# Optimization experiments

Hardware: AMD Instinct MI355X
Metric: run time of the kernel (lower is better)

The kernel has to match this reference:

```python
import jax, jax.numpy as jnp
import numpy as np

B, SQ, SK, D = 8, 512, 512, 32


def _spd_cov(key, b, s, d):
    # random SPD covariance: A A^T + I
    a = 0.1 * jax.random.normal(key, (b, s, d, d), dtype=jnp.float32)
    return jnp.einsum('bsde,bsfe->bsdf', a, a) + jnp.eye(d, dtype=jnp.float32)


def setup_inputs() -> dict:
    key = jax.random.key(0)
    ks = jax.random.split(key, 6)
    return {
        'q_mean': jax.random.normal(ks[0], (B, SQ, D), dtype=jnp.float32),
        'q_cov': _spd_cov(ks[1], B, SQ, D),
        'k_mean': jax.random.normal(ks[2], (B, SK, D), dtype=jnp.float32),
        'k_cov': _spd_cov(ks[3], B, SK, D),
        'v_mean': jax.random.normal(ks[4], (B, SK, D), dtype=jnp.float32),
        'v_cov': _spd_cov(ks[5], B, SK, D),
    }


def reference(q_mean, q_cov, k_mean, k_cov, v_mean, v_cov):
    # Pairwise symmetric Gaussian JSD attention.
    # JSD = 0.5*(KL(p_q||p_k)+KL(p_k||p_q)); the log-det terms cancel:
    # JSD = 0.25*( tr(Sk^-1 Sq) + tr(Sq^-1 Sk) - 2D
    #              + dm^T (Sk^-1 + Sq^-1) dm ),  dm = mu_q - mu_k
    d = q_mean.shape[-1]
    q_inv = jnp.linalg.inv(q_cov)            # [B,Sq,D,D]
    k_inv = jnp.linalg.inv(k_cov)            # [B,Sk,D,D]
    tr_kq = jnp.einsum('bkde,bqed->bqk', k_inv, q_cov)
    tr_qk = jnp.einsum('bqde,bked->bqk', q_inv, k_cov)
    dm = q_mean[:, :, None, :] - k_mean[:, None, :, :]   # [B,Sq,Sk,D]
    quad = (jnp.einsum('bqkd,bkde,bqke->bqk', dm, k_inv, dm)
            + jnp.einsum('bqkd,bqde,bqke->bqk', dm, q_inv, dm))
    js = 0.25 * (tr_kq + tr_qk - 2.0 * d + quad)         # [B,Sq,Sk]
    score = jax.nn.softmax(js, axis=-1)
    out_mean = jnp.einsum('bqk,bkd->bqd', score, v_mean)
    out_cov = jnp.einsum('bqk,bkde->bqde', score, v_cov)
    return out_mean, out_cov
```

## Files before the change

### kernel.cpp

```cpp
#include <hip/hip_runtime.h>
#include <hip/hip_bf16.h>

#define NBATCH 8
#define SQL 512
#define SKL 512
#define DD 32
#define KF 1152
#define UT 528
#define NOUT 1056
#define NVT 1088
#define NSITE (NBATCH * SQL)
#define VS_BLOCKS (34 * 16 * NBATCH)

typedef short short8 __attribute__((ext_vector_type(8)));
typedef float f32x4 __attribute__((ext_vector_type(4)));
typedef unsigned short ushort_t;

__device__ __forceinline__ ushort_t f2bf(float f) {
    unsigned int u = __float_as_uint(f);
    return (ushort_t)((u + 0x7fffu + ((u >> 16) & 1u)) >> 16);
}
__device__ __forceinline__ float bf2f(ushort_t h) {
    return __uint_as_float(((unsigned int)h) << 16);
}
__device__ __forceinline__ void gl_lds16(const ushort_t* g, ushort_t* l) {
    __builtin_amdgcn_global_load_lds(
        (const __attribute__((address_space(1))) void*)g,
        (__attribute__((address_space(3))) void*)l, 16, 0, 0);
}
__device__ __forceinline__ void pk_split(float v0, float v1, ushort_t& h0, ushort_t& h1,
                                         ushort_t& l0, ushort_t& l1) {
    __hip_bfloat162 H = __float22bfloat162_rn(make_float2(v0, v1));
    ushort2 hu = *(ushort2*)&H;
    h0 = hu.x; h1 = hu.y;
    __hip_bfloat162 L = __float22bfloat162_rn(make_float2(v0 - bf2f(hu.x), v1 - bf2f(hu.y)));
    ushort2 lu = *(ushort2*)&L;
    l0 = lu.x; l1 = lu.y;
}

template<int P>
__device__ __forceinline__ float swzb(float x) {
    return __int_as_float(__builtin_amdgcn_ds_swizzle(__float_as_int(x), (P << 5)));
}
template<int M>
__device__ __forceinline__ float swzx(float x) {
    return __int_as_float(__builtin_amdgcn_ds_swizzle(__float_as_int(x), (M << 10) | 0x1F));
}

template<int P>
__device__ __forceinline__ void gj_step(float (&a)[DD], int hl) {
    float piv = swzb<P>(a[P]);
    float rinv = __builtin_amdgcn_rcpf(piv);
    float t = a[P] * rinv;
    bool isp = (hl == P);
    float u = isp ? rinv : t;
    float g = isp ? 0.0f : 1.0f;
    #pragma unroll
    for (int i = 0; i < DD; ++i) {
        if (i == P) continue;
        float ci = swzb<P>(a[i]);
        a[i] = fmaf(a[i], g, -(ci * u));
    }
    a[P] = u;
}
template<int P>
__device__ __forceinline__ void gj_run(float (&a)[DD], int hl) {
    gj_step<P>(a, hl);
    if constexpr (P + 1 < DD) gj_run<P + 1>(a, hl);
}

__global__ __launch_bounds__(256, 4) void feat_kernel(
    const float* __restrict__ qm, const float* __restrict__ qc,
    const float* __restrict__ km, const float* __restrict__ kc,
    ushort_t* __restrict__ fqh, ushort_t* __restrict__ fql,
    ushort_t* __restrict__ fkh, ushort_t* __restrict__ fkl)
{
    __shared__ float inv2[8 * 1064];
    __shared__ float mu2[8 * 32];

    const int tid = threadIdx.x;
    const int wid = tid >> 6, lane = tid & 63;
    const int half = lane >> 5, hl = lane & 31;
    const int site_g = (blockIdx.x * 4 + wid) * 2 + half;
    const int qside = site_g < NSITE;
    const int site = qside ? site_g : site_g - NSITE;

    const float* covp = (qside ? qc : kc) + (size_t)site * (DD * DD);
    const float* mup  = (qside ? qm : km) + (size_t)site * DD;
    ushort_t* fh = qside ? fqh : fkh;
    ushort_t* fl = qside ? fql : fkl;
    const size_t fo = (size_t)site * KF;

    float* inv_s = inv2 + (wid * 2 + half) * 1064;
    float* mu_s  = mu2 + (wid * 2 + half) * 32;

    const float mu_lane = mup[hl];
    mu_s[hl] = mu_lane;

    float a[DD];
    #pragma unroll
    for (int r = 0; r < DD; ++r) a[r] = covp[r * DD + hl];

    gj_run<0>(a, hl);

    #pragma unroll
    for (int r = 0; r < DD; ++r) inv_s[r * 33 + hl] = a[r];

    float ivr = 0.f;
    #pragma unroll
    for (int e = 0; e < DD; ++e) ivr = fmaf(a[e], mu_s[e], ivr);

    float pb = mu_lane * ivr;
    pb += swzx<1>(pb); pb += swzx<2>(pb); pb += swzx<4>(pb);
    pb += swzx<8>(pb); pb += swzx<16>(pb);
    const float bias = pb;

    for (int idx = hl; idx < UT; idx += 32) {
        int d = (int)((65.0f - sqrtf(4225.0f - 8.0f * (float)idx)) * 0.5f);
        if (d > 0 && (d * (65 - d)) / 2 > idx) --d;
        if (((d + 1) * (64 - d)) / 2 <= idx) ++d;
        int off = (d * (65 - d)) / 2;
        int e = d + (idx - off);
        float Mv = covp[d * DD + e] + mu_s[d] * mu_s[e];
        float Iv = inv_s[d * 33 + e];
        float w = (d == e) ? 0.25f : 0.5f;
        float v0, v1;
        if (qside) { v0 = w * Mv; v1 = w * Iv; }
        else       { v0 = Iv;     v1 = Mv; }
        ushort_t h0, h1, l0, l1;
        pk_split(v0, v1, h0, h1, l0, l1);
        fh[fo + idx] = h0; fh[fo + UT + idx] = h1;
        fl[fo + idx] = l0; fl[fo + UT + idx] = l1;
    }
    {
        float v0, v1;
        if (qside) { v0 = -0.5f * ivr; v1 = 0.25f * mu_lane; }
        else       { v0 = mu_lane;     v1 = -2.f * ivr; }
        ushort_t h0, h1, l0, l1;
        pk_split(v0, v1, h0, h1, l0, l1);
        fh[fo + 2*UT + hl] = h0; fh[fo + 2*UT + DD + hl] = h1;
        fl[fo + 2*UT + hl] = l0; fl[fo + 2*UT + DD + hl] = l1;
    }
    if (hl == 0) {
        float v = qside ? 0.25f : bias;
        ushort_t hb = f2bf(v);
        fh[fo + 2*UT + 2*DD] = hb;
        fl[fo + 2*UT + 2*DD] = f2bf(v - bf2f(hb));
    }
    for (int i = 2*UT + 2*DD + 1 + hl; i < KF; i += 32) { fh[fo + i] = 0; fl[fo + i] = 0; }
}

template<int MODE>
__global__ __launch_bounds__(256) void gemm_split(
    const ushort_t* __restrict__ Ah_g, const ushort_t* __restrict__ Al_g,
    const ushort_t* __restrict__ Bh_g, const ushort_t* __restrict__ Bl_g,
    float* __restrict__ C0, float* __restrict__ C1)
{
    constexpr bool SPLIT = (MODE == 0);
    constexpr int KSTRIDE = SPLIT ? KF : SKL;
    constexpr int KITERS = SPLIT ? (KF / 2 / 32) : (SKL / 32);
    const int b = blockIdx.z, nt = blockIdx.x;
    const int mt = SPLIT ? (blockIdx.y & 3) : blockIdx.y;
    const int kbase = SPLIT ? ((blockIdx.y >> 2) * (KF / 2)) : 0;
    const int tid = threadIdx.x, lane = tid & 63, wid = tid >> 6;
    const int wm = wid & 1, wn = wid >> 1;
    const int BROWS = MODE ? NVT : SKL;

    const ushort_t* Ah = Ah_g + ((size_t)b * SQL + mt * 128) * KSTRIDE;
    const ushort_t* Al = Al_g + ((size_t)b * SQL + mt * 128) * KSTRIDE;
    const ushort_t* Bh = Bh_g + ((size_t)b * BROWS + nt * 64) * KSTRIDE;
    const ushort_t* Bl = Bl_g + ((size_t)b * BROWS + nt * 64) * KSTRIDE;

    __shared__ __align__(16) ushort_t AsH[128 * 32];
    __shared__ __align__(16) ushort_t AsL[SPLIT ? 128 * 32 : 8];
    __shared__ __align__(16) ushort_t BsH[64 * 32];
    __shared__ __align__(16) ushort_t BsL[SPLIT ? 64 * 32 : 8];

    const int r4 = lane >> 2, kp = (lane & 3) * 8;
    const int arow0 = wid * 16 + r4,        aoff0 = wid * 512 + lane * 8;
    const int arow1 = (wid + 4) * 16 + r4,  aoff1 = (wid + 4) * 512 + lane * 8;

    const int fm = lane & 15;
    const int q8 = (lane >> 4) * 8;

    f32x4 acc[4][2];
    #pragma unroll
    for (int i = 0; i < 4; ++i)
        #pragma unroll
        for (int j = 0; j < 2; ++j)
            acc[i][j] = (f32x4){0.f, 0.f, 0.f, 0.f};

    for (int it = 0; it < KITERS; ++it) {
        const int k0 = kbase + it * 32;
        __syncthreads();
        gl_lds16(Ah + (size_t)arow0 * KSTRIDE + k0 + kp, &AsH[aoff0]);
        gl_lds16(Ah + (size_t)arow1 * KSTRIDE + k0 + kp, &AsH[aoff1]);
        gl_lds16(Bh + (size_t)arow0 * KSTRIDE + k0 + kp, &BsH[aoff0]);
        if (SPLIT) {
            gl_lds16(Al + (size_t)arow0 * KSTRIDE + k0 + kp, &AsL[aoff0]);
            gl_lds16(Al + (size_t)arow1 * KSTRIDE + k0 + kp, &AsL[aoff1]);
            gl_lds16(Bl + (size_t)arow0 * KSTRIDE + k0 + kp, &BsL[aoff0]);
        }
        __syncthreads();

        short8 ah[4], al[4], bh[2], bl[2];
        #pragma unroll
        for (int i = 0; i < 4; ++i) {
            const int r = wm * 64 + i * 16 + fm;
            ah[i] = *(const short8*)&AsH[r * 32 + q8];
            if (SPLIT) al[i] = *(const short8*)&AsL[r * 32 + q8];
        }
        #pragma unroll
        for (int j = 0; j < 2; ++j) {
            const int r = wn * 32 + j * 16 + fm;
            bh[j] = *(const short8*)&BsH[r * 32 + q8];
            if (SPLIT) bl[j] = *(const short8*)&BsL[r * 32 + q8];
        }
        #pragma unroll
        for (int i = 0; i < 4; ++i)
            #pragma unroll
            for (int j = 0; j < 2; ++j) {
                acc[i][j] = __builtin_amdgcn_mfma_f32_16x16x32_bf16(ah[i], bh[j], acc[i][j], 0, 0, 0);
                if (SPLIT) {
                    acc[i][j] = __builtin_amdgcn_mfma_f32_16x16x32_bf16(ah[i], bl[j], acc[i][j], 0, 0, 0);
                    acc[i][j] = __builtin_amdgcn_mfma_f32_16x16x32_bf16(al[i], bh[j], acc[i][j], 0, 0, 0);
                }
            }
    }

    const int crow0 = (lane >> 4) * 4;
    const int ccol = lane & 15;
    #pragma unroll
    for (int i = 0; i < 4; ++i) {
        const int m = mt * 128 + wm * 64 + i * 16 + crow0;
        #pragma unroll
        for (int j = 0; j < 2; ++j) {
            const int n = nt * 64 + wn * 32 + j * 16 + ccol;
            #pragma unroll
            for (int r = 0; r < 4; ++r) {
                const float v = acc[i][j][r];
                const size_t rowb = (size_t)b * SQL + (m + r);
                if (MODE == 0) {
                    atomicAdd(&C0[rowb * SKL + n], v);
                } else {
                    if (n < DD)        C0[rowb * DD + n] = v;
                    else if (n < NOUT) C1[rowb * (DD * DD) + (n - DD)] = v;
                }
            }
        }
    }
}

__global__ __launch_bounds__(256) void phase2_kernel(
    const float* __restrict__ js, ushort_t* __restrict__ ph,
    const float* __restrict__ vmean, const float* __restrict__ vcov,
    ushort_t* __restrict__ vth)
{
    __shared__ float sm[32 * 33];
    const int tid = threadIdx.x;
    if (blockIdx.x < (unsigned)(NBATCH * SQL)) {
        const float* p = js + (size_t)blockIdx.x * SKL;
        float2 v = *(const float2*)(p + 2 * tid);
        float m = fmaxf(v.x, v.y);
        #pragma unroll
        for (int o = 32; o > 0; o >>= 1) m = fmaxf(m, __shfl_xor(m, o));
        const int wid = tid >> 6, ln = tid & 63;
        if (ln == 0) sm[wid] = m;
        __syncthreads();
        m = fmaxf(fmaxf(sm[0], sm[1]), fmaxf(sm[2], sm[3]));
        float e0 = __expf(v.x - m), e1 = __expf(v.y - m);
        float s = e0 + e1;
        #pragma unroll
        for (int o = 32; o > 0; o >>= 1) s += __shfl_xor(s, o);
        if (ln == 0) sm[4 + wid] = s;
        __syncthreads();
        s = sm[4] + sm[5] + sm[6] + sm[7];
        float rs = 1.0f / s;
        size_t o = (size_t)blockIdx.x * SKL + 2 * tid;
        ph[o]     = f2bf(e0 * rs);
        ph[o + 1] = f2bf(e1 * rs);
    } else {
        const int vb = blockIdx.x - NBATCH * SQL;
        const int b = vb / (34 * 16), rem = vb % (34 * 16);
        const int kt = rem / 34, nt = rem % 34;
        const int n0 = nt * 32, k0 = kt * 32;
        const int tx = tid & 31, ty = tid >> 5;
        for (int r = ty; r < 32; r += 8) {
            const int k = k0 + r, n = n0 + tx;
            float v;
            if (n0 == 0)          v = vmean[((size_t)b * SKL + k) * DD + n];
            else if (n0 >= NOUT)  v = 0.f;
            else                  v = vcov[((size_t)b * SKL + k) * (DD * DD) + (n - DD)];
            sm[tx * 33 + r] = v;
        }
        __syncthreads();
        for (int r = ty; r < 32; r += 8) {
            const int n = n0 + r, k = k0 + tx;
            vth[((size_t)b * NVT + n) * SKL + k] = f2bf(sm[r * 33 + tx]);
        }
    }
}

extern "C" void kernel_launch(void* const* d_in, const int* in_sizes, int n_in,
                              void* d_out, int out_size, void* d_ws, size_t ws_size,
                              hipStream_t stream)
{
    const float* q_mean = (const float*)d_in[0];
    const float* q_cov  = (const float*)d_in[1];
    const float* k_mean = (const float*)d_in[2];
    const float* k_cov  = (const float*)d_in[3];
    const float* v_mean = (const float*)d_in[4];
    const float* v_cov  = (const float*)d_in[5];

    float* out_mean = (float*)d_out;
    float* out_cov  = out_mean + (size_t)NBATCH * SQL * DD;

    char* w = (char*)d_ws;
    const size_t FQN = (size_t)NBATCH * SQL * KF;
    ushort_t* fq_h = (ushort_t*)w;
    ushort_t* fq_l = fq_h + FQN;
    ushort_t* fk_h = fq_l + FQN;
    ushort_t* fk_l = fk_h + FQN;
    float*    js   = (float*)(fk_l + FQN);
    ushort_t* vt_h = fq_h;
    ushort_t* p_h  = fk_h;

    feat_kernel<<<2 * NSITE / 8, 256, 0, stream>>>(
        q_mean, q_cov, k_mean, k_cov, fq_h, fq_l, fk_h, fk_l);
    hipMemsetAsync(js, 0, (size_t)NBATCH * SQL * SKL * sizeof(float), stream);
    gemm_split<0><<<dim3(SKL / 64, 8, NBATCH), 256, 0, stream>>>(
        fq_h, fq_l, fk_h, fk_l, js, nullptr);
    phase2_kernel<<<NBATCH * SQL + VS_BLOCKS, 256, 0, stream>>>(
        js, p_h, v_mean, v_cov, vt_h);
    gemm_split<1><<<dim3(NVT / 64, SQL / 128, NBATCH), 256, 0, stream>>>(
        p_h, nullptr, vt_h, nullptr, out_mean, out_cov);
}
```

Before: 190.3 us.

## Replace split-K atomics with dual partial buffers and pack inverse in LDS

The split-K feature GEMM writes each K-half to its own score buffer with plain stores. This removes the memset and the atomicAdd traffic, and the softmax kernel sums the two partials on load. The path is chosen at runtime only when the workspace is large enough, otherwise the old atomic path runs. Separately, feat_kernel stores just the upper triangle of the inverse in packed LDS, which cuts shared memory per block so occupancy can be raised to 8 blocks per CU. The cost is a second score buffer and an extra read in the softmax kernel.

New measurement: 191.5 us. Within noise of the previous version (+0.6%).

```diff
diff --git a/kernel.cpp b/kernel.cpp
--- a/kernel.cpp
+++ b/kernel.cpp
@@ -69,14 +69,13 @@
     if constexpr (P + 1 < DD) gj_run<P + 1>(a, hl);
 }
 
-__global__ __launch_bounds__(256, 4) void feat_kernel(
+__global__ __launch_bounds__(256, 8) void feat_kernel(
     const float* __restrict__ qm, const float* __restrict__ qc,
     const float* __restrict__ km, const float* __restrict__ kc,
     ushort_t* __restrict__ fqh, ushort_t* __restrict__ fql,
     ushort_t* __restrict__ fkh, ushort_t* __restrict__ fkl)
 {
-    __shared__ float inv2[8 * 1064];
-    __shared__ float mu2[8 * 32];
+    __shared__ float smem[8 * 560];
 
     const int tid = threadIdx.x;
     const int wid = tid >> 6, lane = tid & 63;
@@ -91,8 +90,8 @@
     ushort_t* fl = qside ? fql : fkl;
     const size_t fo = (size_t)site * KF;
 
-    float* inv_s = inv2 + (wid * 2 + half) * 1064;
-    float* mu_s  = mu2 + (wid * 2 + half) * 32;
+    float* inv_p = smem + (wid * 2 + half) * 560;
+    float* mu_s  = inv_p + 528;
 
     const float mu_lane = mup[hl];
     mu_s[hl] = mu_lane;
@@ -104,7 +103,8 @@
     gj_run<0>(a, hl);
 
     #pragma unroll
-    for (int r = 0; r < DD; ++r) inv_s[r * 33 + hl] = a[r];
+    for (int r = 0; r < DD; ++r)
+        if (r <= hl) inv_p[((r * (65 - r)) >> 1) + hl - r] = a[r];
 
     float ivr = 0.f;
     #pragma unroll
@@ -122,7 +122,7 @@
         int off = (d * (65 - d)) / 2;
         int e = d + (idx - off);
         float Mv = covp[d * DD + e] + mu_s[d] * mu_s[e];
-        float Iv = inv_s[d * 33 + e];
+        float Iv = inv_p[idx];
         float w = (d == e) ? 0.25f : 0.5f;
         float v0, v1;
         if (qside) { v0 = w * Mv; v1 = w * Iv; }
@@ -150,7 +150,7 @@
     for (int i = 2*UT + 2*DD + 1 + hl; i < KF; i += 32) { fh[fo + i] = 0; fl[fo + i] = 0; }
 }
 
-template<int MODE>
+template<int MODE, int DUAL>
 __global__ __launch_bounds__(256) void gemm_split(
     const ushort_t* __restrict__ Ah_g, const ushort_t* __restrict__ Al_g,
     const ushort_t* __restrict__ Bh_g, const ushort_t* __restrict__ Bl_g,
@@ -161,7 +161,8 @@
     constexpr int KITERS = SPLIT ? (KF / 2 / 32) : (SKL / 32);
     const int b = blockIdx.z, nt = blockIdx.x;
     const int mt = SPLIT ? (blockIdx.y & 3) : blockIdx.y;
-    const int kbase = SPLIT ? ((blockIdx.y >> 2) * (KF / 2)) : 0;
+    const int ks = SPLIT ? (blockIdx.y >> 2) : 0;
+    const int kbase = ks * (SPLIT ? (KF / 2) : 0);
     const int tid = threadIdx.x, lane = tid & 63, wid = tid >> 6;
     const int wm = wid & 1, wn = wid >> 1;
     const int BROWS = MODE ? NVT : SKL;
@@ -228,6 +229,7 @@
             }
     }
 
+    float* Cs = (SPLIT && DUAL && ks) ? C1 : C0;
     const int crow0 = (lane >> 4) * 4;
     const int ccol = lane & 15;
     #pragma unroll
@@ -241,7 +243,8 @@
                 const float v = acc[i][j][r];
                 const size_t rowb = (size_t)b * SQL + (m + r);
                 if (MODE == 0) {
-                    atomicAdd(&C0[rowb * SKL + n], v);
+                    if (DUAL) Cs[rowb * SKL + n] = v;
+                    else      atomicAdd(&C0[rowb * SKL + n], v);
                 } else {
                     if (n < DD)        C0[rowb * DD + n] = v;
                     else if (n < NOUT) C1[rowb * (DD * DD) + (n - DD)] = v;
@@ -251,16 +254,22 @@
     }
 }
 
+template<int DUAL>
 __global__ __launch_bounds__(256) void phase2_kernel(
-    const float* __restrict__ js, ushort_t* __restrict__ ph,
+    const float* __restrict__ js0, const float* __restrict__ js1,
+    ushort_t* __restrict__ ph,
     const float* __restrict__ vmean, const float* __restrict__ vcov,
     ushort_t* __restrict__ vth)
 {
     __shared__ float sm[32 * 33];
     const int tid = threadIdx.x;
     if (blockIdx.x < (unsigned)(NBATCH * SQL)) {
-        const float* p = js + (size_t)blockIdx.x * SKL;
-        float2 v = *(const float2*)(p + 2 * tid);
+        const size_t ro = (size_t)blockIdx.x * SKL + 2 * tid;
+        float2 v = *(const float2*)(js0 + ro);
+        if (DUAL) {
+            float2 v1 = *(const float2*)(js1 + ro);
+            v.x += v1.x; v.y += v1.y;
+        }
         float m = fmaxf(v.x, v.y);
         #pragma unroll
         for (int o = 32; o > 0; o >>= 1) m = fmaxf(m, __shfl_xor(m, o));
@@ -276,9 +285,8 @@
         __syncthreads();
         s = sm[4] + sm[5] + sm[6] + sm[7];
         float rs = 1.0f / s;
-        size_t o = (size_t)blockIdx.x * SKL + 2 * tid;
-        ph[o]     = f2bf(e0 * rs);
-        ph[o + 1] = f2bf(e1 * rs);
+        ph[ro]     = f2bf(e0 * rs);
+        ph[ro + 1] = f2bf(e1 * rs);
     } else {
         const int vb = blockIdx.x - NBATCH * SQL;
         const int b = vb / (34 * 16), rem = vb % (34 * 16);
@@ -317,21 +325,32 @@
 
     char* w = (char*)d_ws;
     const size_t FQN = (size_t)NBATCH * SQL * KF;
+    const size_t JSN = (size_t)NBATCH * SQL * SKL;
     ushort_t* fq_h = (ushort_t*)w;
     ushort_t* fq_l = fq_h + FQN;
     ushort_t* fk_h = fq_l + FQN;
     ushort_t* fk_l = fk_h + FQN;
-    float*    js   = (float*)(fk_l + FQN);
+    float*    js0  = (float*)(fk_l + FQN);
+    float*    js1  = js0 + JSN;
     ushort_t* vt_h = fq_h;
     ushort_t* p_h  = fk_h;
 
+    const bool dual = ws_size >= (8 * FQN + 8 * JSN);
+
     feat_kernel<<<2 * NSITE / 8, 256, 0, stream>>>(
         q_mean, q_cov, k_mean, k_cov, fq_h, fq_l, fk_h, fk_l);
-    hipMemsetAsync(js, 0, (size_t)NBATCH * SQL * SKL * sizeof(float), stream);
-    gemm_split<0><<<dim3(SKL / 64, 8, NBATCH), 256, 0, stream>>>(
-        fq_h, fq_l, fk_h, fk_l, js, nullptr);
-    phase2_kernel<<<NBATCH * SQL + VS_BLOCKS, 256, 0, stream>>>(
-        js, p_h, v_mean, v_cov, vt_h);
-    gemm_split<1><<<dim3(NVT / 64, SQL / 128, NBATCH), 256, 0, stream>>>(
+    if (dual) {
+        gemm_split<0, 1><<<dim3(SKL / 64, 8, NBATCH), 256, 0, stream>>>(
+            fq_h, fq_l, fk_h, fk_l, js0, js1);
+        phase2_kernel<1><<<NBATCH * SQL + VS_BLOCKS, 256, 0, stream>>>(
+            js0, js1, p_h, v_mean, v_cov, vt_h);
+    } else {
+        hipMemsetAsync(js0, 0, JSN * sizeof(float), stream);
+        gemm_split<0, 0><<<dim3(SKL / 64, 8, NBATCH), 256, 0, stream>>>(
+            fq_h, fq_l, fk_h, fk_l, js0, nullptr);
+        phase2_kernel<0><<<NBATCH * SQL + VS_BLOCKS, 256, 0, stream>>>(
+            js0, nullptr, p_h, v_mean, v_cov, vt_h);
+    }
+    gemm_split<1, 0><<<dim3(NVT / 64, SQL / 128, NBATCH), 256, 0, stream>>>(
         p_h, nullptr, vt_h, nullptr, out_mean, out_cov);
 }
```
